# Optimization experiments

Measured on AMD Instinct MI355X. Metric: run time of the kernel, lower is better.

## Reference

```python
import jax, jax.numpy as jnp
import numpy as np

B, S, D_MODEL, N_HEADS = 2, 2048, 1024, 16
HEAD_DIM = D_MODEL // N_HEADS  # 64
SCALE = HEAD_DIM ** -0.5
MASK_FILL = -1e9


def setup_inputs() -> dict:
    key = jax.random.key(0)
    k1, k2, k3 = jax.random.split(key, 3)
    x = jax.random.normal(k1, (B, S, D_MODEL), dtype=jnp.float32)
    # nn.Linear weight [3*d_att, d_model], trunc_normal std=0.02 style init
    W_qkv = jax.random.normal(k2, (3 * D_MODEL, D_MODEL), dtype=jnp.float32) * 0.02
    # boolean attention mask over the full [b, s_q, h, t_k] score tensor (True = keep)
    mask = jax.random.bernoulli(k3, p=0.9, shape=(B, S, N_HEADS, S))
    return {"x": x, "W_qkv": W_qkv, "mask": mask}


def reference(x, W_qkv, mask):
    b, s, dm = x.shape
    h, d = N_HEADS, HEAD_DIM
    # fused QKV projection (no bias): [b,s,3*dm] -> [b,s,3,h,d]
    qkv = jnp.einsum('bsm,nm->bsn', x, W_qkv).reshape(b, s, 3, h, d)
    q, k, v = qkv[:, :, 0], qkv[:, :, 1], qkv[:, :, 2]
    # scores: [b, s_q, h, t_k]
    attn = jnp.einsum('bshd,bthd->bsht', q, k) * SCALE
    attn = jnp.where(mask, attn, MASK_FILL)
    attn = jax.nn.softmax(attn, axis=-1)
    # out[b,t,h,d] = sum_s attn[b,t,h,s] * v[b,s,h,d]  (original einsum 'b s h d, b t h s -> b t h d')
    out = jnp.einsum('bshd,bths->bthd', v, attn)
    return out.reshape(b, s, h * d)  # proj is Identity (d_out=None)
```

## Files before the change

### kernel.cpp

```cpp
#include <hip/hip_runtime.h>

#define S_   2048
#define DM_  1024
#define NH_  16
#define HD_  64
#define KDIM 1024
#define QB_  128

typedef __attribute__((ext_vector_type(8))) short  shortx8;
typedef __attribute__((ext_vector_type(4))) float  floatx4;

#define AS1 __attribute__((address_space(1)))
#define AS3 __attribute__((address_space(3)))

__device__ __forceinline__ unsigned short f2bf(float f) {
  unsigned u = __float_as_uint(f);
  u += 0x7FFFu + ((u >> 16) & 1u);
  return (unsigned short)(u >> 16);
}

__device__ __forceinline__ void gld_lds16(const void* g, unsigned short* l) {
  __builtin_amdgcn_global_load_lds((const AS1 void*)g, (AS3 void*)l, 16, 0, 0);
}

__global__ __launch_bounds__(256) void qkv_gemm(const void* __restrict__ Xv,
                                                const void* __restrict__ Wv,
                                                unsigned short* __restrict__ Qg,
                                                unsigned short* __restrict__ Kg,
                                                unsigned short* __restrict__ Vt)
{
  __shared__ unsigned short lA[128*64];
  __shared__ unsigned short lB[128*64];
  __shared__ int sx;
  const int tid  = threadIdx.x;
  const int wid  = tid >> 6,  lane = tid & 63;
  const int quad = lane >> 4, l16  = lane & 15;
  const int bm = blockIdx.x, bn = blockIdx.y;
  const int wM = (wid >> 1) * 64, wN = (wid & 1) * 64;

  if (tid == 0) sx = 0;
  __syncthreads();
  {
    unsigned xv = ((const unsigned*)Xv)[tid];
    unsigned b1 = (xv >> 8) & 0x7Fu;
    bool pb = (b1 >= 0x32u && b1 <= 0x41u);
    unsigned long long bal = __ballot(pb);
    if (lane == 0) atomicAdd(&sx, (int)__popcll(bal));
  }
  __syncthreads();
  const int xbf = sx > 128;

  floatx4 acc[4][4] = {};

  for (int kt = 0; kt < KDIM; kt += 64) {
    __syncthreads();
    if (xbf) {
      const unsigned short* X = (const unsigned short*)Xv;
      const unsigned short* W = (const unsigned short*)Wv;
      #pragma unroll
      for (int p = 0; p < 4; ++p) {
        int chunk = p*256 + tid;
        int r = chunk >> 3, c = chunk & 7;
        gld_lds16(X + (size_t)(bm*128 + r)*KDIM + kt + c*8, lA + chunk*8);
      }
      #pragma unroll
      for (int p = 0; p < 4; ++p) {
        int chunk = p*256 + tid;
        int r = chunk >> 3, c = chunk & 7;
        gld_lds16(W + (size_t)(bn*128 + r)*KDIM + kt + c*8, lB + chunk*8);
      }
    } else {
      const float* X = (const float*)Xv;
      const float* W = (const float*)Wv;
      #pragma unroll
      for (int p = 0; p < 8; ++p) {
        int c4 = p*256 + tid;
        int r = c4 >> 4, c = c4 & 15;
        float4 v = *(const float4*)(X + (size_t)(bm*128 + r)*KDIM + kt + c*4);
        unsigned short* d = lA + r*64 + c*4;
        d[0]=f2bf(v.x); d[1]=f2bf(v.y); d[2]=f2bf(v.z); d[3]=f2bf(v.w);
      }
      #pragma unroll
      for (int p = 0; p < 8; ++p) {
        int c4 = p*256 + tid;
        int r = c4 >> 4, c = c4 & 15;
        float4 v = *(const float4*)(W + (size_t)(bn*128 + r)*KDIM + kt + c*4);
        unsigned short* d = lB + r*64 + c*4;
        d[0]=f2bf(v.x); d[1]=f2bf(v.y); d[2]=f2bf(v.z); d[3]=f2bf(v.w);
      }
    }
    __syncthreads();

    #pragma unroll
    for (int ks = 0; ks < 2; ++ks) {
      shortx8 af[4], bfr[4];
      #pragma unroll
      for (int mi = 0; mi < 4; ++mi)
        af[mi] = *(const shortx8*)(lA + (wM + mi*16 + l16)*64 + ks*32 + quad*8);
      #pragma unroll
      for (int ni = 0; ni < 4; ++ni)
        bfr[ni] = *(const shortx8*)(lB + (wN + ni*16 + l16)*64 + ks*32 + quad*8);
      #pragma unroll
      for (int mi = 0; mi < 4; ++mi)
        #pragma unroll
        for (int ni = 0; ni < 4; ++ni)
          acc[mi][ni] = __builtin_amdgcn_mfma_f32_16x16x32_bf16(af[mi], bfr[ni], acc[mi][ni], 0, 0, 0);
    }
  }

  if (bn < 8) {
    #pragma unroll
    for (int mi = 0; mi < 4; ++mi)
      #pragma unroll
      for (int ni = 0; ni < 4; ++ni)
        #pragma unroll
        for (int r = 0; r < 4; ++r) {
          int m = bm*128 + wM + mi*16 + quad*4 + r;
          int n = bn*128 + wN + ni*16 + l16;
          int b = m >> 11, q = m & 2047, h = n >> 6, d = n & 63;
          Qg[(((size_t)(b*NH_ + h))*S_ + q)*HD_ + d] = f2bf(acc[mi][ni][r] * 0.125f);
        }
  } else if (bn < 16) {
    #pragma unroll
    for (int mi = 0; mi < 4; ++mi)
      #pragma unroll
      for (int ni = 0; ni < 4; ++ni)
        #pragma unroll
        for (int r = 0; r < 4; ++r) {
          int m = bm*128 + wM + mi*16 + quad*4 + r;
          int n = bn*128 + wN + ni*16 + l16 - 1024;
          int b = m >> 11, t = m & 2047, h = n >> 6, d = n & 63;
          Kg[(((size_t)(b*NH_ + h))*S_ + t)*HD_ + d] = f2bf(acc[mi][ni][r]);
        }
  } else {
    #pragma unroll
    for (int mi = 0; mi < 4; ++mi)
      #pragma unroll
      for (int ni = 0; ni < 4; ++ni) {
        int m0 = bm*128 + wM + mi*16 + quad*4;
        int n  = bn*128 + wN + ni*16 + l16 - 2048;
        int b = m0 >> 11, t = m0 & 2047, h = n >> 6, d = n & 63;
        ushort4 u;
        u.x = f2bf(acc[mi][ni][0]); u.y = f2bf(acc[mi][ni][1]);
        u.z = f2bf(acc[mi][ni][2]); u.w = f2bf(acc[mi][ni][3]);
        *(ushort4*)(Vt + (((size_t)(b*NH_ + h))*HD_ + d)*S_ + t) = u;
      }
  }
}

__global__ __launch_bounds__(256, 2) void attn_kernel(const unsigned short* __restrict__ Qg,
                                                      const unsigned short* __restrict__ Kg,
                                                      const unsigned short* __restrict__ Vt,
                                                      const void* __restrict__ maskp,
                                                      const void* __restrict__ xg,
                                                      void* __restrict__ outv)
{
  __shared__ unsigned short lQ[QB_*HD_];
  __shared__ unsigned short lK[2][64*HD_];
  __shared__ unsigned short lVt[2][HD_*64];
  __shared__ int sdet[5];

  const int tid  = threadIdx.x;
  const int wid  = tid >> 6,  lane = tid & 63;
  const int quad = lane >> 4, l16  = lane & 15;
  const int qb = blockIdx.x * QB_;
  const int h  = blockIdx.y, b = blockIdx.z;
  const int bh = b*NH_ + h;

  if (tid < 5) sdet[tid] = (tid == 4) ? 0 : 1;
  __syncthreads();
  {
    unsigned mv = ((const unsigned*)maskp)[tid];
    bool o32  = (mv <= 1u);
    bool of32 = (mv == 0u) || (mv == 0x3F800000u);
    unsigned lo = mv & 0xFFFFu, hi = mv >> 16;
    bool o16 = ((lo==0u)||(lo==0x3F80u)) && ((hi==0u)||(hi==0x3F80u));
    bool o8  = ((mv & 0xFEFEFEFEu) == 0u);
    unsigned xv = ((const unsigned*)xg)[tid];
    unsigned b1 = (xv >> 8) & 0x7Fu;
    bool pb = (b1 >= 0x32u && b1 <= 0x41u);
    unsigned long long B0 = __ballot(o32), B1 = __ballot(of32);
    unsigned long long B2 = __ballot(o16), B3 = __ballot(o8);
    unsigned long long BX = __ballot(pb);
    if (lane == 0) {
      if (~B0) atomicAnd(&sdet[0], 0);
      if (~B1) atomicAnd(&sdet[1], 0);
      if (~B2) atomicAnd(&sdet[2], 0);
      if (~B3) atomicAnd(&sdet[3], 0);
      atomicAdd(&sdet[4], (int)__popcll(BX));
    }
  }

  #pragma unroll
  for (int p = 0; p < 4; ++p) {
    int chunk = p*256 + tid;
    gld_lds16(Qg + ((size_t)bh*S_ + qb)*HD_ + chunk*8, lQ + chunk*8);
  }

  auto stage = [&](int t0, int buf) {
    #pragma unroll
    for (int p = 0; p < 2; ++p) {
      int chunk = p*256 + tid;
      gld_lds16(Kg + ((size_t)bh*S_ + t0)*HD_ + chunk*8, lK[buf] + chunk*8);
    }
    #pragma unroll
    for (int p = 0; p < 2; ++p) {
      int chunk = p*256 + tid;
      int r = chunk >> 3, c = chunk & 7;
      gld_lds16(Vt + ((size_t)bh*HD_ + r)*S_ + t0 + c*8, lVt[buf] + chunk*8);
    }
  };

  size_t mrow[2][4];
  #pragma unroll
  for (int qh = 0; qh < 2; ++qh)
    #pragma unroll
    for (int r = 0; r < 4; ++r) {
      int q = qb + wid*32 + qh*16 + quad*4 + r;
      mrow[qh][r] = (((size_t)b*S_ + q)*NH_ + h)*S_ + l16;
    }

  stage(0, 0);
  __syncthreads();

  const int mflag = sdet[0] ? 0 : (sdet[1] ? 3 : (sdet[2] ? 2 : 1));
  const int obf   = sdet[4] > 128;

  auto loadraw = [&](int t0, unsigned (*mz)[4][4]) {
    if (mflag == 1) {
      const unsigned char* mp = (const unsigned char*)maskp;
      #pragma unroll
      for (int qh = 0; qh < 2; ++qh)
        #pragma unroll
        for (int r = 0; r < 4; ++r)
          #pragma unroll
          for (int tile = 0; tile < 4; ++tile) mz[qh][r][tile] = mp[mrow[qh][r] + t0 + tile*16];
    } else if (mflag == 2) {
      const unsigned short* mp = (const unsigned short*)maskp;
      #pragma unroll
      for (int qh = 0; qh < 2; ++qh)
        #pragma unroll
        for (int r = 0; r < 4; ++r)
          #pragma unroll
          for (int tile = 0; tile < 4; ++tile) mz[qh][r][tile] = mp[mrow[qh][r] + t0 + tile*16];
    } else {
      const unsigned* mp = (const unsigned*)maskp;
      #pragma unroll
      for (int qh = 0; qh < 2; ++qh)
        #pragma unroll
        for (int r = 0; r < 4; ++r)
          #pragma unroll
          for (int tile = 0; tile < 4; ++tile) mz[qh][r][tile] = mp[mrow[qh][r] + t0 + tile*16];
    }
  };

  shortx8 qf[2][2];
  #pragma unroll
  for (int qh = 0; qh < 2; ++qh)
    #pragma unroll
    for (int ks = 0; ks < 2; ++ks)
      qf[qh][ks] = *(const shortx8*)(lQ + (wid*32 + qh*16 + l16)*HD_ + ks*32 + quad*8);

  floatx4 acc[2][4] = {};
  float lsum[2][4] = {};
  unsigned short* lPw = lQ + wid*2048;

  unsigned mc = 0;
  {
    unsigned m0[2][4][4];
    loadraw(0, m0);
    #pragma unroll
    for (int qh = 0; qh < 2; ++qh)
      #pragma unroll
      for (int r = 0; r < 4; ++r)
        #pragma unroll
        for (int tile = 0; tile < 4; ++tile)
          mc |= (m0[qh][r][tile] != 0u ? 1u : 0u) << (qh*16 + r*4 + tile);
  }

  for (int t0 = 0; t0 < S_; t0 += 64) {
    const int cur = (t0 >> 6) & 1;
    unsigned mraw[2][4][4];
    const bool more = (t0 + 64 < S_);
    if (more) {
      stage(t0 + 64, cur ^ 1);
      loadraw(t0 + 64, mraw);
    }

    #pragma unroll
    for (int qh = 0; qh < 2; ++qh) {
      floatx4 sc[4] = {};
      #pragma unroll
      for (int tile = 0; tile < 4; ++tile)
        #pragma unroll
        for (int ks = 0; ks < 2; ++ks) {
          shortx8 kf = *(const shortx8*)(lK[cur] + (tile*16 + l16)*64 + ks*32 + quad*8);
          sc[tile] = __builtin_amdgcn_mfma_f32_16x16x32_bf16(qf[qh][ks], kf, sc[tile], 0, 0, 0);
        }

      #pragma unroll
      for (int tile = 0; tile < 4; ++tile)
        #pragma unroll
        for (int r = 0; r < 4; ++r) {
          float e = __expf(sc[tile][r]);
          e = (mc & (1u << (qh*16 + r*4 + tile))) ? e : 0.f;
          lsum[qh][r] += e;
          int row = qh*16 + quad*4 + r;
          int col = tile*16 + l16;
          lPw[(row << 6) + (((col >> 3) ^ (row & 7)) << 3) + (col & 7)] = f2bf(e);
        }

      #pragma unroll
      for (int ks = 0; ks < 2; ++ks) {
        int prow = qh*16 + l16;
        shortx8 pa = *(const shortx8*)(lPw + (prow << 6) + (((ks*4 + quad) ^ (prow & 7)) << 3));
        #pragma unroll
        for (int d = 0; d < 4; ++d) {
          shortx8 vb = *(const shortx8*)(lVt[cur] + (d*16 + l16)*64 + ks*32 + quad*8);
          acc[qh][d] = __builtin_amdgcn_mfma_f32_16x16x32_bf16(pa, vb, acc[qh][d], 0, 0, 0);
        }
      }
    }

    unsigned mcn = 0;
    if (more) {
      #pragma unroll
      for (int qh = 0; qh < 2; ++qh)
        #pragma unroll
        for (int r = 0; r < 4; ++r)
          #pragma unroll
          for (int tile = 0; tile < 4; ++tile)
            mcn |= (mraw[qh][r][tile] != 0u ? 1u : 0u) << (qh*16 + r*4 + tile);
    }
    __syncthreads();
    mc = mcn;
  }

  float rinv[2][4];
  #pragma unroll
  for (int qh = 0; qh < 2; ++qh)
    #pragma unroll
    for (int r = 0; r < 4; ++r) {
      float l = lsum[qh][r];
      #pragma unroll
      for (int o = 1; o < 16; o <<= 1) l += __shfl_xor(l, o);
      rinv[qh][r] = 1.f / l;
    }

  #pragma unroll
  for (int qh = 0; qh < 2; ++qh)
    #pragma unroll
    for (int d = 0; d < 4; ++d)
      #pragma unroll
      for (int r = 0; r < 4; ++r) {
        int q = qb + wid*32 + qh*16 + quad*4 + r;
        size_t oi = ((size_t)b*S_ + q)*DM_ + h*HD_ + d*16 + l16;
        float v = acc[qh][d][r] * rinv[qh][r];
        if (obf) ((unsigned short*)outv)[oi] = f2bf(v);
        else     ((float*)outv)[oi]          = v;
      }
}

extern "C" void kernel_launch(void* const* d_in, const int* in_sizes, int n_in,
                              void* d_out, int out_size, void* d_ws, size_t ws_size,
                              hipStream_t stream) {
  (void)in_sizes; (void)n_in; (void)out_size; (void)ws_size;
  const void* X    = d_in[0];
  const void* W    = d_in[1];
  const void* mask = d_in[2];
  const size_t SEG = (size_t)2*NH_*S_*HD_*2;
  unsigned short* Qg = (unsigned short*)((char*)d_ws + 256);
  unsigned short* Kg = (unsigned short*)((char*)d_ws + 256 + SEG);
  unsigned short* Vt = (unsigned short*)((char*)d_ws + 256 + 2*SEG);

  qkv_gemm<<<dim3(32, 24), 256, 0, stream>>>(X, W, Qg, Kg, Vt);
  attn_kernel<<<dim3(S_/QB_, NH_, 2), 256, 0, stream>>>(Qg, Kg, Vt, mask, X, d_out);
}
```

Baseline: 851.1 us.

## Pre-convert X and W to bf16, interleave attention MFMAs, raise occupancy

Adds a separate conversion kernel that writes bf16 copies of X and W to workspace. The GEMM can then always stage tiles with direct global-to-LDS loads instead of converting fp32 inside every K-tile, at the cost of an extra launch and extra memory traffic. In the attention kernel, the two query halves' QK and PV MFMAs are interleaved so each K/V fragment loaded from LDS is reused twice. The occupancy hint goes from 2 to 3 blocks per CU, and mask element-size detection is simplified.

```diff
diff --git a/kernel.cpp b/kernel.cpp
--- a/kernel.cpp
+++ b/kernel.cpp
@@ -23,21 +23,13 @@
   __builtin_amdgcn_global_load_lds((const AS1 void*)g, (AS3 void*)l, 16, 0, 0);
 }
 
-__global__ __launch_bounds__(256) void qkv_gemm(const void* __restrict__ Xv,
-                                                const void* __restrict__ Wv,
-                                                unsigned short* __restrict__ Qg,
-                                                unsigned short* __restrict__ Kg,
-                                                unsigned short* __restrict__ Vt)
+__global__ __launch_bounds__(256) void convert_xw(const void* __restrict__ Xv,
+                                                  const void* __restrict__ Wv,
+                                                  unsigned short* __restrict__ Xb,
+                                                  unsigned short* __restrict__ Wb)
 {
-  __shared__ unsigned short lA[128*64];
-  __shared__ unsigned short lB[128*64];
   __shared__ int sx;
-  const int tid  = threadIdx.x;
-  const int wid  = tid >> 6,  lane = tid & 63;
-  const int quad = lane >> 4, l16  = lane & 15;
-  const int bm = blockIdx.x, bn = blockIdx.y;
-  const int wM = (wid >> 1) * 64, wN = (wid & 1) * 64;
-
+  const int tid = threadIdx.x, lane = tid & 63;
   if (tid == 0) sx = 0;
   __syncthreads();
   {
@@ -48,46 +40,57 @@
     if (lane == 0) atomicAdd(&sx, (int)__popcll(bal));
   }
   __syncthreads();
-  const int xbf = sx > 128;
+  const bool xbf = sx > 128;
+
+  const size_t GX = (size_t)4096*1024/8;
+  const size_t GT = GX + (size_t)3072*1024/8;
+  for (size_t g = (size_t)blockIdx.x*256 + tid; g < GT; g += (size_t)gridDim.x*256) {
+    const bool isX = g < GX;
+    const size_t e = (isX ? g : g - GX) * 8;
+    const void* src = isX ? Xv : Wv;
+    unsigned short* dst = isX ? Xb : Wb;
+    if (xbf) {
+      *(uint4*)(dst + e) = *(const uint4*)((const unsigned short*)src + e);
+    } else {
+      float4 a = *(const float4*)((const float*)src + e);
+      float4 b = *(const float4*)((const float*)src + e + 4);
+      ushort4 u0{f2bf(a.x), f2bf(a.y), f2bf(a.z), f2bf(a.w)};
+      ushort4 u1{f2bf(b.x), f2bf(b.y), f2bf(b.z), f2bf(b.w)};
+      *(ushort4*)(dst + e)     = u0;
+      *(ushort4*)(dst + e + 4) = u1;
+    }
+  }
+}
+
+__global__ __launch_bounds__(256) void qkv_gemm(const unsigned short* __restrict__ Xb,
+                                                const unsigned short* __restrict__ Wb,
+                                                unsigned short* __restrict__ Qg,
+                                                unsigned short* __restrict__ Kg,
+                                                unsigned short* __restrict__ Vt)
+{
+  __shared__ unsigned short lA[128*64];
+  __shared__ unsigned short lB[128*64];
+  const int tid  = threadIdx.x;
+  const int wid  = tid >> 6,  lane = tid & 63;
+  const int quad = lane >> 4, l16  = lane & 15;
+  const int bm = blockIdx.x, bn = blockIdx.y;
+  const int wM = (wid >> 1) * 64, wN = (wid & 1) * 64;
 
   floatx4 acc[4][4] = {};
 
   for (int kt = 0; kt < KDIM; kt += 64) {
     __syncthreads();
-    if (xbf) {
-      const unsigned short* X = (const unsigned short*)Xv;
-      const unsigned short* W = (const unsigned short*)Wv;
-      #pragma unroll
-      for (int p = 0; p < 4; ++p) {
-        int chunk = p*256 + tid;
-        int r = chunk >> 3, c = chunk & 7;
-        gld_lds16(X + (size_t)(bm*128 + r)*KDIM + kt + c*8, lA + chunk*8);
-      }
-      #pragma unroll
-      for (int p = 0; p < 4; ++p) {
-        int chunk = p*256 + tid;
-        int r = chunk >> 3, c = chunk & 7;
-        gld_lds16(W + (size_t)(bn*128 + r)*KDIM + kt + c*8, lB + chunk*8);
-      }
-    } else {
-      const float* X = (const float*)Xv;
-      const float* W = (const float*)Wv;
-      #pragma unroll
-      for (int p = 0; p < 8; ++p) {
-        int c4 = p*256 + tid;
-        int r = c4 >> 4, c = c4 & 15;
-        float4 v = *(const float4*)(X + (size_t)(bm*128 + r)*KDIM + kt + c*4);
-        unsigned short* d = lA + r*64 + c*4;
-        d[0]=f2bf(v.x); d[1]=f2bf(v.y); d[2]=f2bf(v.z); d[3]=f2bf(v.w);
-      }
-      #pragma unroll
-      for (int p = 0; p < 8; ++p) {
-        int c4 = p*256 + tid;
-        int r = c4 >> 4, c = c4 & 15;
-        float4 v = *(const float4*)(W + (size_t)(bn*128 + r)*KDIM + kt + c*4);
-        unsigned short* d = lB + r*64 + c*4;
-        d[0]=f2bf(v.x); d[1]=f2bf(v.y); d[2]=f2bf(v.z); d[3]=f2bf(v.w);
-      }
+    #pragma unroll
+    for (int p = 0; p < 4; ++p) {
+      int chunk = p*256 + tid;
+      int r = chunk >> 3, c = chunk & 7;
+      gld_lds16(Xb + (size_t)(bm*128 + r)*KDIM + kt + c*8, lA + chunk*8);
+    }
+    #pragma unroll
+    for (int p = 0; p < 4; ++p) {
+      int chunk = p*256 + tid;
+      int r = chunk >> 3, c = chunk & 7;
+      gld_lds16(Wb + (size_t)(bn*128 + r)*KDIM + kt + c*8, lB + chunk*8);
     }
     __syncthreads();
 
@@ -148,7 +151,7 @@
   }
 }
 
-__global__ __launch_bounds__(256, 2) void attn_kernel(const unsigned short* __restrict__ Qg,
+__global__ __launch_bounds__(256, 3) void attn_kernel(const unsigned short* __restrict__ Qg,
                                                       const unsigned short* __restrict__ Kg,
                                                       const unsigned short* __restrict__ Vt,
                                                       const void* __restrict__ maskp,
@@ -158,7 +161,7 @@
   __shared__ unsigned short lQ[QB_*HD_];
   __shared__ unsigned short lK[2][64*HD_];
   __shared__ unsigned short lVt[2][HD_*64];
-  __shared__ int sdet[5];
+  __shared__ int sdet[3];
 
   const int tid  = threadIdx.x;
   const int wid  = tid >> 6,  lane = tid & 63;
@@ -167,27 +170,21 @@
   const int h  = blockIdx.y, b = blockIdx.z;
   const int bh = b*NH_ + h;
 
-  if (tid < 5) sdet[tid] = (tid == 4) ? 0 : 1;
+  if (tid < 3) sdet[tid] = (tid == 2) ? 0 : 1;
   __syncthreads();
   {
     unsigned mv = ((const unsigned*)maskp)[tid];
-    bool o32  = (mv <= 1u);
-    bool of32 = (mv == 0u) || (mv == 0x3F800000u);
+    bool w4 = (mv <= 1u) || (mv == 0x3F800000u);
     unsigned lo = mv & 0xFFFFu, hi = mv >> 16;
-    bool o16 = ((lo==0u)||(lo==0x3F80u)) && ((hi==0u)||(hi==0x3F80u));
-    bool o8  = ((mv & 0xFEFEFEFEu) == 0u);
+    bool w2 = ((lo==0u)||(lo==0x3F80u)) && ((hi==0u)||(hi==0x3F80u));
     unsigned xv = ((const unsigned*)xg)[tid];
     unsigned b1 = (xv >> 8) & 0x7Fu;
     bool pb = (b1 >= 0x32u && b1 <= 0x41u);
-    unsigned long long B0 = __ballot(o32), B1 = __ballot(of32);
-    unsigned long long B2 = __ballot(o16), B3 = __ballot(o8);
-    unsigned long long BX = __ballot(pb);
+    unsigned long long B4 = __ballot(w4), B2 = __ballot(w2), BX = __ballot(pb);
     if (lane == 0) {
-      if (~B0) atomicAnd(&sdet[0], 0);
-      if (~B1) atomicAnd(&sdet[1], 0);
-      if (~B2) atomicAnd(&sdet[2], 0);
-      if (~B3) atomicAnd(&sdet[3], 0);
-      atomicAdd(&sdet[4], (int)__popcll(BX));
+      if (~B4) atomicAnd(&sdet[0], 0);
+      if (~B2) atomicAnd(&sdet[1], 0);
+      atomicAdd(&sdet[2], (int)__popcll(BX));
     }
   }
 
@@ -222,20 +219,19 @@
 
   stage(0, 0);
   __syncthreads();
-
-  const int mflag = sdet[0] ? 0 : (sdet[1] ? 3 : (sdet[2] ? 2 : 1));
-  const int obf   = sdet[4] > 128;
+  const int esz = sdet[0] ? 4 : (sdet[1] ? 2 : 1);
+  const int obf = sdet[2] > 128;
 
   auto loadraw = [&](int t0, unsigned (*mz)[4][4]) {
-    if (mflag == 1) {
-      const unsigned char* mp = (const unsigned char*)maskp;
+    if (esz == 4) {
+      const unsigned* mp = (const unsigned*)maskp;
       #pragma unroll
       for (int qh = 0; qh < 2; ++qh)
         #pragma unroll
         for (int r = 0; r < 4; ++r)
           #pragma unroll
           for (int tile = 0; tile < 4; ++tile) mz[qh][r][tile] = mp[mrow[qh][r] + t0 + tile*16];
-    } else if (mflag == 2) {
+    } else if (esz == 2) {
       const unsigned short* mp = (const unsigned short*)maskp;
       #pragma unroll
       for (int qh = 0; qh < 2; ++qh)
@@ -244,7 +240,7 @@
           #pragma unroll
           for (int tile = 0; tile < 4; ++tile) mz[qh][r][tile] = mp[mrow[qh][r] + t0 + tile*16];
     } else {
-      const unsigned* mp = (const unsigned*)maskp;
+      const unsigned char* mp = (const unsigned char*)maskp;
       #pragma unroll
       for (int qh = 0; qh < 2; ++qh)
         #pragma unroll
@@ -287,22 +283,23 @@
       loadraw(t0 + 64, mraw);
     }
 
-    #pragma unroll
-    for (int qh = 0; qh < 2; ++qh) {
-      floatx4 sc[4] = {};
-      #pragma unroll
-      for (int tile = 0; tile < 4; ++tile)
-        #pragma unroll
-        for (int ks = 0; ks < 2; ++ks) {
-          shortx8 kf = *(const shortx8*)(lK[cur] + (tile*16 + l16)*64 + ks*32 + quad*8);
-          sc[tile] = __builtin_amdgcn_mfma_f32_16x16x32_bf16(qf[qh][ks], kf, sc[tile], 0, 0, 0);
-        }
-
-      #pragma unroll
-      for (int tile = 0; tile < 4; ++tile)
-        #pragma unroll
-        for (int r = 0; r < 4; ++r) {
-          float e = __expf(sc[tile][r]);
+    floatx4 sc[2][4] = {};
+    #pragma unroll
+    for (int tile = 0; tile < 4; ++tile)
+      #pragma unroll
+      for (int ks = 0; ks < 2; ++ks) {
+        shortx8 kf = *(const shortx8*)(lK[cur] + (tile*16 + l16)*64 + ks*32 + quad*8);
+        sc[0][tile] = __builtin_amdgcn_mfma_f32_16x16x32_bf16(qf[0][ks], kf, sc[0][tile], 0, 0, 0);
+        sc[1][tile] = __builtin_amdgcn_mfma_f32_16x16x32_bf16(qf[1][ks], kf, sc[1][tile], 0, 0, 0);
+      }
+
+    #pragma unroll
+    for (int qh = 0; qh < 2; ++qh)
+      #pragma unroll
+      for (int r = 0; r < 4; ++r)
+        #pragma unroll
+        for (int tile = 0; tile < 4; ++tile) {
+          float e = __expf(sc[qh][tile][r]);
           e = (mc & (1u << (qh*16 + r*4 + tile))) ? e : 0.f;
           lsum[qh][r] += e;
           int row = qh*16 + quad*4 + r;
@@ -310,17 +307,22 @@
           lPw[(row << 6) + (((col >> 3) ^ (row & 7)) << 3) + (col & 7)] = f2bf(e);
         }
 
+    shortx8 pa[2][2];
+    #pragma unroll
+    for (int qh = 0; qh < 2; ++qh)
       #pragma unroll
       for (int ks = 0; ks < 2; ++ks) {
         int prow = qh*16 + l16;
-        shortx8 pa = *(const shortx8*)(lPw + (prow << 6) + (((ks*4 + quad) ^ (prow & 7)) << 3));
-        #pragma unroll
-        for (int d = 0; d < 4; ++d) {
-          shortx8 vb = *(const shortx8*)(lVt[cur] + (d*16 + l16)*64 + ks*32 + quad*8);
-          acc[qh][d] = __builtin_amdgcn_mfma_f32_16x16x32_bf16(pa, vb, acc[qh][d], 0, 0, 0);
-        }
-      }
-    }
+        pa[qh][ks] = *(const shortx8*)(lPw + (prow << 6) + (((ks*4 + quad) ^ (prow & 7)) << 3));
+      }
+    #pragma unroll
+    for (int ks = 0; ks < 2; ++ks)
+      #pragma unroll
+      for (int d = 0; d < 4; ++d) {
+        shortx8 vb = *(const shortx8*)(lVt[cur] + (d*16 + l16)*64 + ks*32 + quad*8);
+        acc[0][d] = __builtin_amdgcn_mfma_f32_16x16x32_bf16(pa[0][ks], vb, acc[0][d], 0, 0, 0);
+        acc[1][d] = __builtin_amdgcn_mfma_f32_16x16x32_bf16(pa[1][ks], vb, acc[1][d], 0, 0, 0);
+      }
 
     unsigned mcn = 0;
     if (more) {
@@ -372,7 +374,10 @@
   unsigned short* Qg = (unsigned short*)((char*)d_ws + 256);
   unsigned short* Kg = (unsigned short*)((char*)d_ws + 256 + SEG);
   unsigned short* Vt = (unsigned short*)((char*)d_ws + 256 + 2*SEG);
-
-  qkv_gemm<<<dim3(32, 24), 256, 0, stream>>>(X, W, Qg, Kg, Vt);
+  unsigned short* Xb = (unsigned short*)((char*)d_ws + 256 + 3*SEG);
+  unsigned short* Wb = Xb + (size_t)4096*1024;
+
+  convert_xw<<<512, 256, 0, stream>>>(X, W, Xb, Wb);
+  qkv_gemm<<<dim3(32, 24), 256, 0, stream>>>(Xb, Wb, Qg, Kg, Vt);
   attn_kernel<<<dim3(S_/QB_, NH_, 2), 256, 0, stream>>>(Qg, Kg, Vt, mask, X, d_out);
 }
```

Result: slower. 1.022 ms (+20.1%).
